# Kernel tuning notes

Measured on AMD Instinct MI355X. Metric: run time of the kernel, lower is better.

Reference implementation:

```python
import jax, jax.numpy as jnp
import numpy as np

N = 524288          # events per batch
NUM_NODES = 1_000_000
D = 64              # memory_dim


def gru_cell(x, h, W_ih, W_hh, b_ih, b_hh):
    # torch.nn.GRUCell math; gates ordered (r, z, n)
    gi = x @ W_ih.T + b_ih          # [N, 3D]
    gh = h @ W_hh.T + b_hh          # [N, 3D]
    i_r, i_z, i_n = jnp.split(gi, 3, axis=-1)
    h_r, h_z, h_n = jnp.split(gh, 3, axis=-1)
    r = jax.nn.sigmoid(i_r + h_r)
    z = jax.nn.sigmoid(i_z + h_z)
    n = jnp.tanh(i_n + r * h_n)
    return (1.0 - z) * n + z * h


def setup_inputs() -> dict:
    key = jax.random.key(0)
    ks = jax.random.split(key, 9)
    scale = 1.0 / np.sqrt(D).astype(np.float32)
    return {
        "node_ids": jax.random.randint(ks[0], (N,), 0, NUM_NODES, dtype=jnp.int64)
        if jax.config.jax_enable_x64 else jax.random.randint(ks[0], (N,), 0, NUM_NODES, dtype=jnp.int32),
        "node_embeddings": jax.random.normal(ks[1], (N, D), jnp.float32),
        "timestamps": jax.random.uniform(ks[2], (N,), jnp.float32) * 1000.0,
        "node_memory": jax.random.normal(ks[3], (NUM_NODES, D), jnp.float32) * 0.1,
        "last_update_time": jax.random.uniform(ks[4], (NUM_NODES,), jnp.float32) * 500.0,
        "W_time": jax.random.normal(ks[5], (1, D), jnp.float32) * 0.1,
        "b_time": jnp.zeros((D,), jnp.float32),
        "W_ih": jax.random.normal(ks[6], (3 * D, D), jnp.float32) * scale,
        "W_hh": jax.random.normal(ks[7], (3 * D, D), jnp.float32) * scale,
        "b_ih": jnp.zeros((3 * D,), jnp.float32),
        "b_hh": jnp.zeros((3 * D,), jnp.float32),
    }


def reference(node_ids, node_embeddings, timestamps, node_memory, last_update_time,
              W_time, b_time, W_ih, W_hh, b_ih, b_hh):
    # gather persistent state
    current_memory = node_memory[node_ids]                          # [N, D]
    time_deltas = timestamps - last_update_time[node_ids]           # [N]
    # nn.Linear(1, D): out = dt * W_time[0] + b_time
    time_encoding = time_deltas[:, None] * W_time[0] + b_time       # [N, D]
    updated_memory = gru_cell(node_embeddings + time_encoding, current_memory,
                              W_ih, W_hh, b_ih, b_hh)               # [N, D]
    # scatter write-back (detached in torch)
    new_node_memory = node_memory.at[node_ids].set(jax.lax.stop_gradient(updated_memory))
    new_last_update_time = last_update_time.at[node_ids].set(jax.lax.stop_gradient(timestamps))
    return updated_memory, new_node_memory, new_last_update_time
```

## Files before the change

### kernel.cpp

```cpp
#include <hip/hip_runtime.h>
#include <cstdint>
#include <cstddef>

#define DD 64

typedef float    f32x4  __attribute__((ext_vector_type(4)));
typedef _Float16 f16x8  __attribute__((ext_vector_type(8)));
typedef _Float16 f16x4  __attribute__((ext_vector_type(4)));

__device__ __forceinline__ float sigmoidf_(float x) {
    return 1.0f / (1.0f + __expf(-x));
}
__device__ __forceinline__ float tanh_fast(float x) {
    float ax = fabsf(x);
    float t = 1.0f - 2.0f / (1.0f + __expf(2.0f * ax));
    return copysignf(t, x);
}
__device__ __forceinline__ f32x4 MFMA(f32x4 c, f16x8 a, f16x8 b) {
    return __builtin_amdgcn_mfma_f32_16x16x32_f16(a, b, c, 0, 0, 0);
}

__global__ void k_prep_init(const float* __restrict__ Wih, const float* __restrict__ Whh,
                            _Float16* __restrict__ bhi, _Float16* __restrict__ blo,
                            int* __restrict__ winner, int num_nodes)
{
    if (blockIdx.x < 16) {
        int f = blockIdx.x * 4 + (threadIdx.x >> 6);
        int l = threadIdx.x & 63;
        int g = f >> 2, s = f & 3;
        int c = g * 16 + (l & 15);
        int grp = c >> 6, dd = c & 63;
        int kbase = s * 32 + (l >> 4) * 8;
        int row = (grp == 0) ? dd : (grp == 1) ? 64 + dd : 128 + dd;

        f16x8 hv, lv;
        for (int j = 0; j < 8; ++j) {
            int k = kbase + j;
            float v;
            if (grp <= 1)      v = (k < 64) ? Wih[row * 64 + k] : Whh[row * 64 + (k - 64)];
            else if (grp == 2) v = (k < 64) ? Wih[row * 64 + k] : 0.0f;
            else               v = (k < 64) ? 0.0f : Whh[row * 64 + (k - 64)];
            _Float16 h = (_Float16)v;
            hv[j] = h;
            lv[j] = (_Float16)(v - (float)h);
        }
        size_t off = ((size_t)f * 64 + l);
        ((f16x8*)bhi)[off] = hv;
        ((f16x8*)blo)[off] = lv;
    } else {
        int i = (int)(blockIdx.x - 16) * 256 + threadIdx.x;
        if (i < num_nodes) winner[i] = -1;
    }
}

__global__ void k_vote_dt(const int* __restrict__ ids, const float* __restrict__ ts,
                          const float* __restrict__ lut, int* __restrict__ winner,
                          float* __restrict__ dtw, int n) {
    int i = blockIdx.x * blockDim.x + threadIdx.x;
    if (i < n) {
        int id = ids[i];
        atomicMax(&winner[id], i);
        dtw[i] = ts[i] - lut[id];
    }
}

__global__ __launch_bounds__(256, 4) void k_gru(
    const int* __restrict__ ids,
    const float* __restrict__ emb,
    const float* __restrict__ mem,
    const float* __restrict__ Wt,
    const float* __restrict__ bt,
    const float* __restrict__ bih,
    const float* __restrict__ bhh,
    const _Float16* __restrict__ bhi,
    const _Float16* __restrict__ blo,
    const int* __restrict__ winner,
    const float* __restrict__ dtw,
    float* __restrict__ out0,
    float* __restrict__ out1,
    int n)
{
    __shared__ _Float16 xhh[64][136];
    __shared__ _Float16 xhl[64][72];
    __shared__ int sid[64];
    __shared__ int swin[64];

    const int w    = threadIdx.x >> 6;
    const int l    = threadIdx.x & 63;
    const int col  = l & 15;
    const int rowg = l >> 4;
    const int d    = w * 16 + col;

    const long base = (long)blockIdx.x * 64;
    const bool full = (base + 64 <= (long)n);

    const int  e16 = w * 16 + col;
    const long evA = base + e16;
    int idA = 0, winA = 0; float dtA = 0.f;
    if (full || evA < n) {
        idA  = ids[evA];
        dtA  = dtw[evA];
        winA = (winner[idA] == (int)evA) ? 1 : 0;
    }
    if (l < 16) { sid[e16] = idA; swin[e16] = winA; }

    f32x4 xv0, xv1, xv2, xv3, hv0, hv1, hv2, hv3;
    float dt0, dt1, dt2, dt3;
    {
        int   i0 = __shfl(idA, 0 * 4 + rowg), i1 = __shfl(idA, 1 * 4 + rowg);
        int   i2 = __shfl(idA, 2 * 4 + rowg), i3 = __shfl(idA, 3 * 4 + rowg);
        dt0 = __shfl(dtA, 0 * 4 + rowg); dt1 = __shfl(dtA, 1 * 4 + rowg);
        dt2 = __shfl(dtA, 2 * 4 + rowg); dt3 = __shfl(dtA, 3 * 4 + rowg);
        const f32x4* emb4 = (const f32x4*)emb;
        const f32x4* mem4 = (const f32x4*)mem;
        const size_t e0 = (size_t)(base + w * 16 + 0 * 4 + rowg) * 16 + col;
        const size_t e1 = (size_t)(base + w * 16 + 1 * 4 + rowg) * 16 + col;
        const size_t e2 = (size_t)(base + w * 16 + 2 * 4 + rowg) * 16 + col;
        const size_t e3 = (size_t)(base + w * 16 + 3 * 4 + rowg) * 16 + col;
        if (full) {
            xv0 = __builtin_nontemporal_load(&emb4[e0]);
            xv1 = __builtin_nontemporal_load(&emb4[e1]);
            xv2 = __builtin_nontemporal_load(&emb4[e2]);
            xv3 = __builtin_nontemporal_load(&emb4[e3]);
            hv0 = mem4[(size_t)i0 * 16 + col];
            hv1 = mem4[(size_t)i1 * 16 + col];
            hv2 = mem4[(size_t)i2 * 16 + col];
            hv3 = mem4[(size_t)i3 * 16 + col];
        } else {
            f32x4 z = {0.f, 0.f, 0.f, 0.f};
            xv0 = xv1 = xv2 = xv3 = hv0 = hv1 = hv2 = hv3 = z;
            if (base + w * 16 + 0 * 4 + rowg < n) { xv0 = emb4[e0]; hv0 = mem4[(size_t)i0 * 16 + col]; }
            if (base + w * 16 + 1 * 4 + rowg < n) { xv1 = emb4[e1]; hv1 = mem4[(size_t)i1 * 16 + col]; }
            if (base + w * 16 + 2 * 4 + rowg < n) { xv2 = emb4[e2]; hv2 = mem4[(size_t)i2 * 16 + col]; }
            if (base + w * 16 + 3 * 4 + rowg < n) { xv3 = emb4[e3]; hv3 = mem4[(size_t)i3 * 16 + col]; }
        }
    }

    const f32x4 wt4 = ((const f32x4*)Wt)[col];
    const f32x4 bt4 = ((const f32x4*)bt)[col];
    {
        #define CONV_WRITE(XV, HV, DT, IT)                                           \
        {                                                                            \
            int r = w * 16 + (IT) * 4 + rowg;                                        \
            f32x4 x = XV;                                                            \
            x.x = fmaf(DT, wt4.x, x.x + bt4.x);                                      \
            x.y = fmaf(DT, wt4.y, x.y + bt4.y);                                      \
            x.z = fmaf(DT, wt4.z, x.z + bt4.z);                                      \
            x.w = fmaf(DT, wt4.w, x.w + bt4.w);                                      \
            f16x4 xh, xl, hh;                                                        \
            _Float16 a;                                                              \
            a = (_Float16)x.x; xh[0] = a; xl[0] = (_Float16)(x.x - (float)a);        \
            a = (_Float16)x.y; xh[1] = a; xl[1] = (_Float16)(x.y - (float)a);        \
            a = (_Float16)x.z; xh[2] = a; xl[2] = (_Float16)(x.z - (float)a);        \
            a = (_Float16)x.w; xh[3] = a; xl[3] = (_Float16)(x.w - (float)a);        \
            hh[0] = (_Float16)(HV).x; hh[1] = (_Float16)(HV).y;                      \
            hh[2] = (_Float16)(HV).z; hh[3] = (_Float16)(HV).w;                      \
            *(f16x4*)&xhh[r][col * 4]      = xh;                                     \
            *(f16x4*)&xhl[r][col * 4]      = xl;                                     \
            *(f16x4*)&xhh[r][64 + col * 4] = hh;                                     \
        }
        CONV_WRITE(xv0, hv0, dt0, 0)
        CONV_WRITE(xv1, hv1, dt1, 1)
        CONV_WRITE(xv2, hv2, dt2, 2)
        CONV_WRITE(xv3, hv3, dt3, 3)
        #undef CONV_WRITE
    }

    const f16x8* H = (const f16x8*)bhi;
    const f16x8* L = (const f16x8*)blo;
    f16x8 BRh0 = H[(size_t)(w * 4 + 0) * 64 + l];
    f16x8 BRh1 = H[(size_t)(w * 4 + 1) * 64 + l];
    f16x8 BRh2 = H[(size_t)(w * 4 + 2) * 64 + l];
    f16x8 BRh3 = H[(size_t)(w * 4 + 3) * 64 + l];
    f16x8 BRl0 = L[(size_t)(w * 4 + 0) * 64 + l];
    f16x8 BRl1 = L[(size_t)(w * 4 + 1) * 64 + l];
    f16x8 BZh0 = H[(size_t)((4 + w) * 4 + 0) * 64 + l];
    f16x8 BZh1 = H[(size_t)((4 + w) * 4 + 1) * 64 + l];
    f16x8 BZh2 = H[(size_t)((4 + w) * 4 + 2) * 64 + l];
    f16x8 BZh3 = H[(size_t)((4 + w) * 4 + 3) * 64 + l];
    f16x8 BZl0 = L[(size_t)((4 + w) * 4 + 0) * 64 + l];
    f16x8 BZl1 = L[(size_t)((4 + w) * 4 + 1) * 64 + l];
    f16x8 BIh0 = H[(size_t)((8 + w) * 4 + 0) * 64 + l];
    f16x8 BIh1 = H[(size_t)((8 + w) * 4 + 1) * 64 + l];
    f16x8 BIl0 = L[(size_t)((8 + w) * 4 + 0) * 64 + l];
    f16x8 BIl1 = L[(size_t)((8 + w) * 4 + 1) * 64 + l];
    f16x8 BHh0 = H[(size_t)((12 + w) * 4 + 2) * 64 + l];
    f16x8 BHh1 = H[(size_t)((12 + w) * 4 + 3) * 64 + l];

    const float bR  = bih[d] + bhh[d];
    const float bZ  = bih[64 + d] + bhh[64 + d];
    const float bIN = bih[128 + d];
    const float bHN = bhh[128 + d];

    __syncthreads();

    #pragma unroll
    for (int mt = 0; mt < 4; ++mt) {
        const int arow = mt * 16 + col;
        const int k0   = rowg * 8;
        f16x8 Ah0 = *(const f16x8*)&xhh[arow][0 * 32 + k0];
        f16x8 Ah1 = *(const f16x8*)&xhh[arow][1 * 32 + k0];
        f16x8 Ah2 = *(const f16x8*)&xhh[arow][2 * 32 + k0];
        f16x8 Ah3 = *(const f16x8*)&xhh[arow][3 * 32 + k0];
        f16x8 Al0 = *(const f16x8*)&xhl[arow][0 * 32 + k0];
        f16x8 Al1 = *(const f16x8*)&xhl[arow][1 * 32 + k0];

        f32x4 aR = {0,0,0,0}, aZ = {0,0,0,0}, aI = {0,0,0,0}, aH = {0,0,0,0};
        __builtin_amdgcn_s_setprio(1);
        aR = MFMA(aR, Ah0, BRh0); aR = MFMA(aR, Ah0, BRl0); aR = MFMA(aR, Al0, BRh0);
        aR = MFMA(aR, Ah1, BRh1); aR = MFMA(aR, Ah1, BRl1); aR = MFMA(aR, Al1, BRh1);
        aR = MFMA(aR, Ah2, BRh2); aR = MFMA(aR, Ah3, BRh3);
        aZ = MFMA(aZ, Ah0, BZh0); aZ = MFMA(aZ, Ah0, BZl0); aZ = MFMA(aZ, Al0, BZh0);
        aZ = MFMA(aZ, Ah1, BZh1); aZ = MFMA(aZ, Ah1, BZl1); aZ = MFMA(aZ, Al1, BZh1);
        aZ = MFMA(aZ, Ah2, BZh2); aZ = MFMA(aZ, Ah3, BZh3);
        aI = MFMA(aI, Ah0, BIh0); aI = MFMA(aI, Ah0, BIl0); aI = MFMA(aI, Al0, BIh0);
        aI = MFMA(aI, Ah1, BIh1); aI = MFMA(aI, Ah1, BIl1); aI = MFMA(aI, Al1, BIh1);
        aH = MFMA(aH, Ah2, BHh0); aH = MFMA(aH, Ah3, BHh1);
        __builtin_amdgcn_s_setprio(0);

        #pragma unroll
        for (int r = 0; r < 4; ++r) {
            int  eloc = mt * 16 + rowg * 4 + r;
            long ev   = base + eloc;
            if (full || ev < n) {
                float rr = sigmoidf_(aR[r] + bR);
                float zz = sigmoidf_(aZ[r] + bZ);
                float nn = tanh_fast(aI[r] + bIN + rr * (aH[r] + bHN));
                float hv = (float)xhh[eloc][64 + d];
                float o  = (1.f - zz) * nn + zz * hv;
                out0[(size_t)ev * 64 + d] = o;
                if (swin[eloc])
                    out1[(size_t)sid[eloc] * 64 + d] = o;
            }
        }
    }
}

__global__ void k_tail(float* out2,
                       const f32x4* __restrict__ mem4,
                       f32x4* __restrict__ out14,
                       const float* __restrict__ ts,
                       const float* __restrict__ lut,
                       int num_nodes)
{
    int idx = blockIdx.x * blockDim.x + threadIdx.x;
    if (idx >= num_nodes * 16) return;
    int nidx = idx >> 4;
    int c    = idx & 15;
    int wv = reinterpret_cast<const int*>(out2)[nidx];
    if (wv < 0) {
        f32x4 v = __builtin_nontemporal_load(&mem4[idx]);
        __builtin_nontemporal_store(v, &out14[idx]);
    }
    if (c == 0) out2[nidx] = (wv >= 0) ? ts[wv] : lut[nidx];
}

extern "C" void kernel_launch(void* const* d_in, const int* in_sizes, int n_in,
                              void* d_out, int out_size, void* d_ws, size_t ws_size,
                              hipStream_t stream) {
    const int*   ids = (const int*)  d_in[0];
    const float* emb = (const float*)d_in[1];
    const float* ts  = (const float*)d_in[2];
    const float* mem = (const float*)d_in[3];
    const float* lut = (const float*)d_in[4];
    const float* Wt  = (const float*)d_in[5];
    const float* bt  = (const float*)d_in[6];
    const float* Wih = (const float*)d_in[7];
    const float* Whh = (const float*)d_in[8];
    const float* bih = (const float*)d_in[9];
    const float* bhh = (const float*)d_in[10];

    const int N         = in_sizes[0];
    const int NUM_NODES = in_sizes[4];

    float* out0 = (float*)d_out;
    float* out1 = out0 + (size_t)N * DD;
    float* out2 = out1 + (size_t)NUM_NODES * DD;
    int*   winner = (int*)out2;

    _Float16* bfragH = (_Float16*)d_ws;
    _Float16* bfragL = bfragH + 64 * 64 * 8;
    float*    dtw    = (float*)((char*)d_ws + 128 * 1024);

    int initBlocks = (NUM_NODES + 255) / 256;
    k_prep_init<<<16 + initBlocks, 256, 0, stream>>>(Wih, Whh, bfragH, bfragL,
                                                     winner, NUM_NODES);
    k_vote_dt<<<(N + 255) / 256, 256, 0, stream>>>(ids, ts, lut, winner, dtw, N);

    int nchunks = (N + 63) / 64;
    k_gru<<<nchunks, 256, 0, stream>>>(ids, emb, mem, Wt, bt, bih, bhh,
                                       bfragH, bfragL, winner, dtw, out0, out1, N);

    long vec = (long)NUM_NODES * 16;
    k_tail<<<(int)((vec + 255) / 256), 256, 0, stream>>>(
        out2, (const f32x4*)mem, (f32x4*)out1, ts, lut, NUM_NODES);
}
```

Baseline: 226.8 us.

## Drop split-fp16 compensation and fold time encoding into gate biases

Removes the hi/lo fp16 split for both the weights and the x activations, so each gate uses plain single-fp16 MFMAs. This cuts the MFMA count by nearly half and removes the xhl shared buffer. The time encoding is applied algebraically: W_ih·(dt·Wt + bt) is precomputed as vectors u and c, and the gate pre-activations get dt·u + c added. The embedding loads are also issued before the id-dependent gathers to overlap latency. Accuracy drops because the x input and the weights now lose their fp16 residual terms, which could matter under tolerance checks.

```diff
diff --git a/kernel.cpp b/kernel.cpp
--- a/kernel.cpp
+++ b/kernel.cpp
@@ -21,34 +21,43 @@
 }
 
 __global__ void k_prep_init(const float* __restrict__ Wih, const float* __restrict__ Whh,
-                            _Float16* __restrict__ bhi, _Float16* __restrict__ blo,
+                            const float* __restrict__ Wt, const float* __restrict__ bt,
+                            _Float16* __restrict__ bhi, float* __restrict__ u, float* __restrict__ c,
                             int* __restrict__ winner, int num_nodes)
 {
     if (blockIdx.x < 16) {
         int f = blockIdx.x * 4 + (threadIdx.x >> 6);
         int l = threadIdx.x & 63;
         int g = f >> 2, s = f & 3;
-        int c = g * 16 + (l & 15);
-        int grp = c >> 6, dd = c & 63;
+        int cc = g * 16 + (l & 15);
+        int grp = cc >> 6, dd = cc & 63;
         int kbase = s * 32 + (l >> 4) * 8;
         int row = (grp == 0) ? dd : (grp == 1) ? 64 + dd : 128 + dd;
 
-        f16x8 hv, lv;
+        f16x8 hv;
         for (int j = 0; j < 8; ++j) {
             int k = kbase + j;
             float v;
             if (grp <= 1)      v = (k < 64) ? Wih[row * 64 + k] : Whh[row * 64 + (k - 64)];
             else if (grp == 2) v = (k < 64) ? Wih[row * 64 + k] : 0.0f;
             else               v = (k < 64) ? 0.0f : Whh[row * 64 + (k - 64)];
-            _Float16 h = (_Float16)v;
-            hv[j] = h;
-            lv[j] = (_Float16)(v - (float)h);
-        }
-        size_t off = ((size_t)f * 64 + l);
-        ((f16x8*)bhi)[off] = hv;
-        ((f16x8*)blo)[off] = lv;
+            hv[j] = (_Float16)v;
+        }
+        ((f16x8*)bhi)[(size_t)f * 64 + l] = hv;
+    } else if (blockIdx.x == 16) {
+        int t = threadIdx.x;
+        if (t < 192) {
+            float su = 0.f, sc = 0.f;
+            for (int k = 0; k < 64; ++k) {
+                float wv = Wih[t * 64 + k];
+                su = fmaf(wv, Wt[k], su);
+                sc = fmaf(wv, bt[k], sc);
+            }
+            u[t] = su;
+            c[t] = sc;
+        }
     } else {
-        int i = (int)(blockIdx.x - 16) * 256 + threadIdx.x;
+        int i = (int)(blockIdx.x - 17) * 256 + threadIdx.x;
         if (i < num_nodes) winner[i] = -1;
     }
 }
@@ -68,12 +77,11 @@
     const int* __restrict__ ids,
     const float* __restrict__ emb,
     const float* __restrict__ mem,
-    const float* __restrict__ Wt,
-    const float* __restrict__ bt,
     const float* __restrict__ bih,
     const float* __restrict__ bhh,
     const _Float16* __restrict__ bhi,
-    const _Float16* __restrict__ blo,
+    const float* __restrict__ u,
+    const float* __restrict__ c,
     const int* __restrict__ winner,
     const float* __restrict__ dtw,
     float* __restrict__ out0,
@@ -81,7 +89,7 @@
     int n)
 {
     __shared__ _Float16 xhh[64][136];
-    __shared__ _Float16 xhl[64][72];
+    __shared__ float sdt[64];
     __shared__ int sid[64];
     __shared__ int swin[64];
 
@@ -94,25 +102,11 @@
     const long base = (long)blockIdx.x * 64;
     const bool full = (base + 64 <= (long)n);
 
-    const int  e16 = w * 16 + col;
-    const long evA = base + e16;
-    int idA = 0, winA = 0; float dtA = 0.f;
-    if (full || evA < n) {
-        idA  = ids[evA];
-        dtA  = dtw[evA];
-        winA = (winner[idA] == (int)evA) ? 1 : 0;
-    }
-    if (l < 16) { sid[e16] = idA; swin[e16] = winA; }
-
-    f32x4 xv0, xv1, xv2, xv3, hv0, hv1, hv2, hv3;
-    float dt0, dt1, dt2, dt3;
+    const f32x4* emb4 = (const f32x4*)emb;
+    const f32x4* mem4 = (const f32x4*)mem;
+
+    f32x4 xv0, xv1, xv2, xv3;
     {
-        int   i0 = __shfl(idA, 0 * 4 + rowg), i1 = __shfl(idA, 1 * 4 + rowg);
-        int   i2 = __shfl(idA, 2 * 4 + rowg), i3 = __shfl(idA, 3 * 4 + rowg);
-        dt0 = __shfl(dtA, 0 * 4 + rowg); dt1 = __shfl(dtA, 1 * 4 + rowg);
-        dt2 = __shfl(dtA, 2 * 4 + rowg); dt3 = __shfl(dtA, 3 * 4 + rowg);
-        const f32x4* emb4 = (const f32x4*)emb;
-        const f32x4* mem4 = (const f32x4*)mem;
         const size_t e0 = (size_t)(base + w * 16 + 0 * 4 + rowg) * 16 + col;
         const size_t e1 = (size_t)(base + w * 16 + 1 * 4 + rowg) * 16 + col;
         const size_t e2 = (size_t)(base + w * 16 + 2 * 4 + rowg) * 16 + col;
@@ -122,74 +116,80 @@
             xv1 = __builtin_nontemporal_load(&emb4[e1]);
             xv2 = __builtin_nontemporal_load(&emb4[e2]);
             xv3 = __builtin_nontemporal_load(&emb4[e3]);
+        } else {
+            f32x4 z = {0.f, 0.f, 0.f, 0.f};
+            xv0 = xv1 = xv2 = xv3 = z;
+            if (base + w * 16 + 0 * 4 + rowg < n) xv0 = emb4[e0];
+            if (base + w * 16 + 1 * 4 + rowg < n) xv1 = emb4[e1];
+            if (base + w * 16 + 2 * 4 + rowg < n) xv2 = emb4[e2];
+            if (base + w * 16 + 3 * 4 + rowg < n) xv3 = emb4[e3];
+        }
+    }
+
+    const int  e16 = w * 16 + col;
+    const long evA = base + e16;
+    int idA = 0, winA = 0; float dtA = 0.f;
+    if (full || evA < n) {
+        idA  = ids[evA];
+        dtA  = dtw[evA];
+        winA = (winner[idA] == (int)evA) ? 1 : 0;
+    }
+    if (l < 16) { sid[e16] = idA; swin[e16] = winA; sdt[e16] = dtA; }
+
+    f32x4 hv0, hv1, hv2, hv3;
+    {
+        int i0 = __shfl(idA, 0 * 4 + rowg), i1 = __shfl(idA, 1 * 4 + rowg);
+        int i2 = __shfl(idA, 2 * 4 + rowg), i3 = __shfl(idA, 3 * 4 + rowg);
+        if (full) {
             hv0 = mem4[(size_t)i0 * 16 + col];
             hv1 = mem4[(size_t)i1 * 16 + col];
             hv2 = mem4[(size_t)i2 * 16 + col];
             hv3 = mem4[(size_t)i3 * 16 + col];
         } else {
             f32x4 z = {0.f, 0.f, 0.f, 0.f};
-            xv0 = xv1 = xv2 = xv3 = hv0 = hv1 = hv2 = hv3 = z;
-            if (base + w * 16 + 0 * 4 + rowg < n) { xv0 = emb4[e0]; hv0 = mem4[(size_t)i0 * 16 + col]; }
-            if (base + w * 16 + 1 * 4 + rowg < n) { xv1 = emb4[e1]; hv1 = mem4[(size_t)i1 * 16 + col]; }
-            if (base + w * 16 + 2 * 4 + rowg < n) { xv2 = emb4[e2]; hv2 = mem4[(size_t)i2 * 16 + col]; }
-            if (base + w * 16 + 3 * 4 + rowg < n) { xv3 = emb4[e3]; hv3 = mem4[(size_t)i3 * 16 + col]; }
-        }
-    }
-
-    const f32x4 wt4 = ((const f32x4*)Wt)[col];
-    const f32x4 bt4 = ((const f32x4*)bt)[col];
-    {
-        #define CONV_WRITE(XV, HV, DT, IT)                                           \
-        {                                                                            \
-            int r = w * 16 + (IT) * 4 + rowg;                                        \
-            f32x4 x = XV;                                                            \
-            x.x = fmaf(DT, wt4.x, x.x + bt4.x);                                      \
-            x.y = fmaf(DT, wt4.y, x.y + bt4.y);                                      \
-            x.z = fmaf(DT, wt4.z, x.z + bt4.z);                                      \
-            x.w = fmaf(DT, wt4.w, x.w + bt4.w);                                      \
-            f16x4 xh, xl, hh;                                                        \
-            _Float16 a;                                                              \
-            a = (_Float16)x.x; xh[0] = a; xl[0] = (_Float16)(x.x - (float)a);        \
-            a = (_Float16)x.y; xh[1] = a; xl[1] = (_Float16)(x.y - (float)a);        \
-            a = (_Float16)x.z; xh[2] = a; xl[2] = (_Float16)(x.z - (float)a);        \
-            a = (_Float16)x.w; xh[3] = a; xl[3] = (_Float16)(x.w - (float)a);        \
-            hh[0] = (_Float16)(HV).x; hh[1] = (_Float16)(HV).y;                      \
-            hh[2] = (_Float16)(HV).z; hh[3] = (_Float16)(HV).w;                      \
-            *(f16x4*)&xhh[r][col * 4]      = xh;                                     \
-            *(f16x4*)&xhl[r][col * 4]      = xl;                                     \
-            *(f16x4*)&xhh[r][64 + col * 4] = hh;                                     \
-        }
-        CONV_WRITE(xv0, hv0, dt0, 0)
-        CONV_WRITE(xv1, hv1, dt1, 1)
-        CONV_WRITE(xv2, hv2, dt2, 2)
-        CONV_WRITE(xv3, hv3, dt3, 3)
-        #undef CONV_WRITE
-    }
+            hv0 = hv1 = hv2 = hv3 = z;
+            if (base + w * 16 + 0 * 4 + rowg < n) hv0 = mem4[(size_t)i0 * 16 + col];
+            if (base + w * 16 + 1 * 4 + rowg < n) hv1 = mem4[(size_t)i1 * 16 + col];
+            if (base + w * 16 + 2 * 4 + rowg < n) hv2 = mem4[(size_t)i2 * 16 + col];
+            if (base + w * 16 + 3 * 4 + rowg < n) hv3 = mem4[(size_t)i3 * 16 + col];
+        }
+    }
+
+    #define CONV_WRITE(XV, HV, IT)                                               \
+    {                                                                            \
+        int r = w * 16 + (IT) * 4 + rowg;                                        \
+        f16x4 xh, hh;                                                            \
+        xh[0] = (_Float16)(XV).x; xh[1] = (_Float16)(XV).y;                      \
+        xh[2] = (_Float16)(XV).z; xh[3] = (_Float16)(XV).w;                      \
+        hh[0] = (_Float16)(HV).x; hh[1] = (_Float16)(HV).y;                      \
+        hh[2] = (_Float16)(HV).z; hh[3] = (_Float16)(HV).w;                      \
+        *(f16x4*)&xhh[r][col * 4]      = xh;                                     \
+        *(f16x4*)&xhh[r][64 + col * 4] = hh;                                     \
+    }
+    CONV_WRITE(xv0, hv0, 0)
+    CONV_WRITE(xv1, hv1, 1)
+    CONV_WRITE(xv2, hv2, 2)
+    CONV_WRITE(xv3, hv3, 3)
+    #undef CONV_WRITE
 
     const f16x8* H = (const f16x8*)bhi;
-    const f16x8* L = (const f16x8*)blo;
     f16x8 BRh0 = H[(size_t)(w * 4 + 0) * 64 + l];
     f16x8 BRh1 = H[(size_t)(w * 4 + 1) * 64 + l];
     f16x8 BRh2 = H[(size_t)(w * 4 + 2) * 64 + l];
     f16x8 BRh3 = H[(size_t)(w * 4 + 3) * 64 + l];
-    f16x8 BRl0 = L[(size_t)(w * 4 + 0) * 64 + l];
-    f16x8 BRl1 = L[(size_t)(w * 4 + 1) * 64 + l];
     f16x8 BZh0 = H[(size_t)((4 + w) * 4 + 0) * 64 + l];
     f16x8 BZh1 = H[(size_t)((4 + w) * 4 + 1) * 64 + l];
     f16x8 BZh2 = H[(size_t)((4 + w) * 4 + 2) * 64 + l];
     f16x8 BZh3 = H[(size_t)((4 + w) * 4 + 3) * 64 + l];
-    f16x8 BZl0 = L[(size_t)((4 + w) * 4 + 0) * 64 + l];
-    f16x8 BZl1 = L[(size_t)((4 + w) * 4 + 1) * 64 + l];
     f16x8 BIh0 = H[(size_t)((8 + w) * 4 + 0) * 64 + l];
     f16x8 BIh1 = H[(size_t)((8 + w) * 4 + 1) * 64 + l];
-    f16x8 BIl0 = L[(size_t)((8 + w) * 4 + 0) * 64 + l];
-    f16x8 BIl1 = L[(size_t)((8 + w) * 4 + 1) * 64 + l];
     f16x8 BHh0 = H[(size_t)((12 + w) * 4 + 2) * 64 + l];
     f16x8 BHh1 = H[(size_t)((12 + w) * 4 + 3) * 64 + l];
 
-    const float bR  = bih[d] + bhh[d];
-    const float bZ  = bih[64 + d] + bhh[64 + d];
-    const float bIN = bih[128 + d];
+    const float uR = u[d],        uZ = u[64 + d],  uI = u[128 + d];
+    const float CR = c[d]        + bih[d]        + bhh[d];
+    const float CZ = c[64 + d]   + bih[64 + d]   + bhh[64 + d];
+    const float CI = c[128 + d]  + bih[128 + d];
     const float bHN = bhh[128 + d];
 
     __syncthreads();
@@ -202,19 +202,14 @@
         f16x8 Ah1 = *(const f16x8*)&xhh[arow][1 * 32 + k0];
         f16x8 Ah2 = *(const f16x8*)&xhh[arow][2 * 32 + k0];
         f16x8 Ah3 = *(const f16x8*)&xhh[arow][3 * 32 + k0];
-        f16x8 Al0 = *(const f16x8*)&xhl[arow][0 * 32 + k0];
-        f16x8 Al1 = *(const f16x8*)&xhl[arow][1 * 32 + k0];
 
         f32x4 aR = {0,0,0,0}, aZ = {0,0,0,0}, aI = {0,0,0,0}, aH = {0,0,0,0};
         __builtin_amdgcn_s_setprio(1);
-        aR = MFMA(aR, Ah0, BRh0); aR = MFMA(aR, Ah0, BRl0); aR = MFMA(aR, Al0, BRh0);
-        aR = MFMA(aR, Ah1, BRh1); aR = MFMA(aR, Ah1, BRl1); aR = MFMA(aR, Al1, BRh1);
+        aR = MFMA(aR, Ah0, BRh0); aR = MFMA(aR, Ah1, BRh1);
         aR = MFMA(aR, Ah2, BRh2); aR = MFMA(aR, Ah3, BRh3);
-        aZ = MFMA(aZ, Ah0, BZh0); aZ = MFMA(aZ, Ah0, BZl0); aZ = MFMA(aZ, Al0, BZh0);
-        aZ = MFMA(aZ, Ah1, BZh1); aZ = MFMA(aZ, Ah1, BZl1); aZ = MFMA(aZ, Al1, BZh1);
+        aZ = MFMA(aZ, Ah0, BZh0); aZ = MFMA(aZ, Ah1, BZh1);
         aZ = MFMA(aZ, Ah2, BZh2); aZ = MFMA(aZ, Ah3, BZh3);
-        aI = MFMA(aI, Ah0, BIh0); aI = MFMA(aI, Ah0, BIl0); aI = MFMA(aI, Al0, BIh0);
-        aI = MFMA(aI, Ah1, BIh1); aI = MFMA(aI, Ah1, BIl1); aI = MFMA(aI, Al1, BIh1);
+        aI = MFMA(aI, Ah0, BIh0); aI = MFMA(aI, Ah1, BIh1);
         aH = MFMA(aH, Ah2, BHh0); aH = MFMA(aH, Ah3, BHh1);
         __builtin_amdgcn_s_setprio(0);
 
@@ -223,9 +218,10 @@
             int  eloc = mt * 16 + rowg * 4 + r;
             long ev   = base + eloc;
             if (full || ev < n) {
-                float rr = sigmoidf_(aR[r] + bR);
-                float zz = sigmoidf_(aZ[r] + bZ);
-                float nn = tanh_fast(aI[r] + bIN + rr * (aH[r] + bHN));
+                float dt = sdt[eloc];
+                float rr = sigmoidf_(aR[r] + fmaf(dt, uR, CR));
+                float zz = sigmoidf_(aZ[r] + fmaf(dt, uZ, CZ));
+                float nn = tanh_fast(aI[r] + fmaf(dt, uI, CI) + rr * (aH[r] + bHN));
                 float hv = (float)xhh[eloc][64 + d];
                 float o  = (1.f - zz) * nn + zz * hv;
                 out0[(size_t)ev * 64 + d] = o;
@@ -246,13 +242,13 @@
     int idx = blockIdx.x * blockDim.x + threadIdx.x;
     if (idx >= num_nodes * 16) return;
     int nidx = idx >> 4;
-    int c    = idx & 15;
+    int cc   = idx & 15;
     int wv = reinterpret_cast<const int*>(out2)[nidx];
     if (wv < 0) {
         f32x4 v = __builtin_nontemporal_load(&mem4[idx]);
         __builtin_nontemporal_store(v, &out14[idx]);
     }
-    if (c == 0) out2[nidx] = (wv >= 0) ? ts[wv] : lut[nidx];
+    if (cc == 0) out2[nidx] = (wv >= 0) ? ts[wv] : lut[nidx];
 }
 
 extern "C" void kernel_launch(void* const* d_in, const int* in_sizes, int n_in,
@@ -279,17 +275,18 @@
     int*   winner = (int*)out2;
 
     _Float16* bfragH = (_Float16*)d_ws;
-    _Float16* bfragL = bfragH + 64 * 64 * 8;
-    float*    dtw    = (float*)((char*)d_ws + 128 * 1024);
+    float*    uvec   = (float*)((char*)d_ws + 64 * 1024);
+    float*    cvec   = uvec + 192;
+    float*    dtw    = (float*)((char*)d_ws + 72 * 1024);
 
     int initBlocks = (NUM_NODES + 255) / 256;
-    k_prep_init<<<16 + initBlocks, 256, 0, stream>>>(Wih, Whh, bfragH, bfragL,
-                                                     winner, NUM_NODES);
+    k_prep_init<<<17 + initBlocks, 256, 0, stream>>>(Wih, Whh, Wt, bt, bfragH,
+                                                     uvec, cvec, winner, NUM_NODES);
     k_vote_dt<<<(N + 255) / 256, 256, 0, stream>>>(ids, ts, lut, winner, dtw, N);
 
     int nchunks = (N + 63) / 64;
-    k_gru<<<nchunks, 256, 0, stream>>>(ids, emb, mem, Wt, bt, bih, bhh,
-                                       bfragH, bfragL, winner, dtw, out0, out1, N);
+    k_gru<<<nchunks, 256, 0, stream>>>(ids, emb, mem, bih, bhh, bfragH,
+                                       uvec, cvec, winner, dtw, out0, out1, N);
 
     long vec = (long)NUM_NODES * 16;
     k_tail<<<(int)((vec + 255) / 256), 256, 0, stream>>>(
```

Result: no change. 225.7 us (-0.5%).
